# Optimization experiments

Hardware: AMD Instinct MI355X
Metric: run time of the kernel (lower is better)

## Reference

```python
import jax, jax.numpy as jnp
import numpy as np

NUM_HEADS = 4
HIDDEN = 128
LN_EPS = 1e-6
NEG_INF = -1e9


def setup_inputs() -> dict:
    key = jax.random.key(0)
    ks = jax.random.split(key, 8)
    B, S, H, NH = 64, 512, HIDDEN, NUM_HEADS
    enc = jax.random.normal(ks[0], (B, S, H), dtype=jnp.float32)
    mask = jax.random.randint(ks[1], (B, 1, S, S), 0, 2, dtype=jnp.int32)
    scale = 1.0 / np.sqrt(H)
    # torch Linear(H, H*NH, bias=False): weight is (H*NH, H); store transposed (H, H*NH)
    Wq = jax.random.normal(ks[2], (H, H * NH), dtype=jnp.float32) * scale
    Wk = jax.random.normal(ks[3], (H, H * NH), dtype=jnp.float32) * scale
    Wv = jax.random.normal(ks[4], (H, H * NH), dtype=jnp.float32) * scale
    Wo = jax.random.normal(ks[5], (H * NH, H), dtype=jnp.float32) * (1.0 / np.sqrt(H * NH))
    gamma = jnp.ones((H,), dtype=jnp.float32)
    beta = jnp.zeros((H,), dtype=jnp.float32)
    return {"enc": enc, "mask": mask, "Wq": Wq, "Wk": Wk, "Wv": Wv, "Wo": Wo, "gamma": gamma, "beta": beta}


def reference(enc, mask, Wq, Wk, Wv, Wo, gamma, beta):
    B, S, H = enc.shape
    NH = NUM_HEADS
    # projections -> (B, NH, S, H): each head has head_dim == hidden_units
    Q = (enc @ Wq).reshape(B, S, NH, H).transpose(0, 2, 1, 3)
    K = (enc @ Wk).reshape(B, S, NH, H).transpose(0, 2, 1, 3)
    V = (enc @ Wv).reshape(B, S, NH, H).transpose(0, 2, 1, 3)
    # scaled dot-product attention with mask (non-flash: full score matrix)
    scores = jnp.einsum('bhqd,bhkd->bhqk', Q, K) / jnp.sqrt(jnp.float32(H))
    scores = jnp.where(mask == 0, jnp.float32(NEG_INF), scores)
    attn = jax.nn.softmax(scores, axis=-1)  # dropout = identity in eval mode
    ctx = jnp.einsum('bhqk,bhkd->bhqd', attn, V)  # (B, NH, S, H)
    ctx = ctx.transpose(0, 2, 1, 3).reshape(B, S, NH * H)
    out = ctx @ Wo + enc  # dropout identity, residual add
    # LayerNorm over last dim
    mu = jnp.mean(out, axis=-1, keepdims=True)
    var = jnp.var(out, axis=-1, keepdims=True)
    return gamma * (out - mu) / jnp.sqrt(var + LN_EPS) + beta
```

## Files before the change

### kernel.cpp

```cpp
#include <hip/hip_runtime.h>
#include <stdint.h>

#define BATCH 64
#define SLEN 512
#define HID 128
#define NHEAD 4
#define DPROJ 512
#define MTOT (BATCH * SLEN)
#define SCALE 0.08838834764831845f
#define LOG2E 1.4426950408889634f

using short8 = __attribute__((ext_vector_type(8))) short;
using f32x4  = __attribute__((ext_vector_type(4))) float;
using u32x4  = __attribute__((ext_vector_type(4))) unsigned int;
using u32x2  = __attribute__((ext_vector_type(2))) unsigned int;
using us4    = __attribute__((ext_vector_type(4))) unsigned short;

__device__ __forceinline__ unsigned short f2bf(float f) {
  unsigned int u = __float_as_uint(f);
  u += 0x7fffu + ((u >> 16) & 1u);
  return (unsigned short)(u >> 16);
}

__global__ __launch_bounds__(256) void prep_kernel(
    const float* __restrict__ Wq,
    const float* __restrict__ Wk,
    const float* __restrict__ Wv,
    const float* __restrict__ Wo,
    const float* __restrict__ enc,
    const int* __restrict__ mask,
    unsigned short* __restrict__ WT,
    unsigned short* __restrict__ WoT,
    unsigned short* __restrict__ encb,
    unsigned int* __restrict__ mbits)
{
  if (blockIdx.x < 1024) {
    int idx = blockIdx.x * 256 + threadIdx.x;
    int z = idx >> 16;
    int i = idx & 65535;
    if (z < 3) {
      const float* W = (z == 0) ? Wq : (z == 1) ? Wk : Wv;
      float scale = (z == 0) ? (SCALE * LOG2E) : 1.0f;
      int k = i >> 9;
      int n = i & 511;
      WT[(size_t)z * 65536 + (size_t)n * 128 + k] = f2bf(W[i] * scale);
    } else {
      int k = i >> 7;
      int n = i & 127;
      WoT[(size_t)n * 512 + k] = f2bf(Wo[i]);
    }
  } else if (blockIdx.x < 3072) {
    size_t tid = (size_t)(blockIdx.x - 1024) * 256 + threadIdx.x;
    const float* s = enc + tid * 8;
    f32x4 a0 = *(const f32x4*)(s);
    f32x4 a1 = *(const f32x4*)(s + 4);
    short8 v;
    #pragma unroll
    for (int j = 0; j < 4; ++j) v[j] = (short)f2bf(a0[j]);
    #pragma unroll
    for (int j = 0; j < 4; ++j) v[4 + j] = (short)f2bf(a1[j]);
    *(short8*)(encb + tid * 8) = v;
  } else {
    const int l = threadIdx.x & 63;
    size_t wavebase = (size_t)(blockIdx.x - 3072) * 1024 + (threadIdx.x >> 6) * 256;
    unsigned long long b0 = __ballot(mask[wavebase + 0 * 64 + l] != 0);
    unsigned long long b1 = __ballot(mask[wavebase + 1 * 64 + l] != 0);
    unsigned long long b2 = __ballot(mask[wavebase + 2 * 64 + l] != 0);
    unsigned long long b3 = __ballot(mask[wavebase + 3 * 64 + l] != 0);
    if (l < 4) {
      unsigned long long v = (l & 2) ? ((l & 1) ? b3 : b2) : ((l & 1) ? b1 : b0);
      *(unsigned long long*)(mbits + (wavebase >> 5) + l * 2) = v;
    }
  }
}

__global__ __launch_bounds__(256) void qkv_kernel(
    const unsigned short* __restrict__ encb,
    const unsigned short* __restrict__ WT,
    unsigned short* __restrict__ Qh,
    unsigned short* __restrict__ Kh,
    unsigned short* __restrict__ Vt)
{
  const int nt = blockIdx.x;
  const int mt = blockIdx.y;
  const int t = threadIdx.x;
  const int lane = t & 63;
  const int w = t >> 6;
  const int quad = lane >> 4;
  const int l16 = lane & 15;

  __shared__ __align__(16) unsigned short Ald[128 * 136];
  __shared__ __align__(16) unsigned short Bld[128 * 72];

  const int m0 = mt * 128, n0 = nt * 128;
  const int wm = (w >> 1) * 64, wn = (w & 1) * 64;

  #pragma unroll
  for (int i = 0; i < 8; ++i) {
    int idx = i * 256 + t;
    int row = idx >> 4;
    int col = (idx & 15) << 3;
    *(u32x4*)(Ald + row * 136 + col) =
        *(const u32x4*)(encb + (size_t)(m0 + row) * HID + col);
  }

  for (int z = 0; z < 3; ++z) {
    const unsigned short* Wz = WT + (size_t)z * DPROJ * HID;

    f32x4 acc[4][4];
    #pragma unroll
    for (int mi = 0; mi < 4; ++mi)
      #pragma unroll
      for (int ni = 0; ni < 4; ++ni)
        acc[mi][ni] = f32x4{0.f, 0.f, 0.f, 0.f};

    #pragma unroll
    for (int kc = 0; kc < 2; ++kc) {
      __syncthreads();
      #pragma unroll
      for (int i = 0; i < 4; ++i) {
        int idx = i * 256 + t;
        int row = idx >> 3;
        int col = (idx & 7) << 3;
        *(u32x4*)(Bld + row * 72 + col) =
            *(const u32x4*)(Wz + (size_t)(n0 + row) * HID + kc * 64 + col);
      }
      __syncthreads();

      #pragma unroll
      for (int kk = 0; kk < 2; ++kk) {
        short8 a[4], bb[4];
        #pragma unroll
        for (int mi = 0; mi < 4; ++mi)
          a[mi] = *(const short8*)(Ald + (wm + mi * 16 + l16) * 136 + kc * 64 + kk * 32 + quad * 8);
        #pragma unroll
        for (int ni = 0; ni < 4; ++ni)
          bb[ni] = *(const short8*)(Bld + (wn + ni * 16 + l16) * 72 + kk * 32 + quad * 8);
        if (z < 2) {
          #pragma unroll
          for (int mi = 0; mi < 4; ++mi)
            #pragma unroll
            for (int ni = 0; ni < 4; ++ni)
              acc[mi][ni] = __builtin_amdgcn_mfma_f32_16x16x32_bf16(bb[ni], a[mi], acc[mi][ni], 0, 0, 0);
        } else {
          #pragma unroll
          for (int mi = 0; mi < 4; ++mi)
            #pragma unroll
            for (int ni = 0; ni < 4; ++ni)
              acc[mi][ni] = __builtin_amdgcn_mfma_f32_16x16x32_bf16(a[mi], bb[ni], acc[mi][ni], 0, 0, 0);
        }
      }
    }

    if (z < 2) {
      unsigned short* outz = ((z == 0) ? Qh : Kh) + (size_t)nt * MTOT * HID;
      #pragma unroll
      for (int mi = 0; mi < 4; ++mi)
        #pragma unroll
        for (int ni = 0; ni < 4; ++ni) {
          int m = m0 + wm + mi * 16 + l16;
          int dbase = wn + ni * 16 + quad * 4;
          us4 pk;
          #pragma unroll
          for (int r = 0; r < 4; ++r) pk[r] = f2bf(acc[mi][ni][r]);
          *(us4*)(outz + (size_t)m * HID + dbase) = pk;
        }
    } else {
      #pragma unroll
      for (int mi = 0; mi < 4; ++mi)
        #pragma unroll
        for (int ni = 0; ni < 4; ++ni) {
          int row0 = m0 + wm + mi * 16 + quad * 4;
          int b = row0 >> 9, s = row0 & 511;
          int d = wn + ni * 16 + l16;
          us4 pk;
          #pragma unroll
          for (int r = 0; r < 4; ++r) pk[r] = f2bf(acc[mi][ni][r]);
          *(us4*)(Vt + ((size_t)(nt * BATCH + b) * HID + d) * SLEN + s) = pk;
        }
    }
  }
}

__global__ __launch_bounds__(512, 4) void attn_kernel(
    const unsigned short* __restrict__ Qh,
    const unsigned short* __restrict__ Kh,
    const unsigned short* __restrict__ Vt,
    const unsigned int* __restrict__ mbits,
    unsigned short* __restrict__ ctx)
{
  const int lin = blockIdx.x;
  const int work = (lin & 7) * 128 + (lin >> 3);
  const int qt = work & 3;
  const int h  = (work >> 2) & 3;
  const int b  = work >> 4;

  const int t = threadIdx.x;
  const int lane = t & 63;
  const int w = t >> 6;
  const int quad = lane >> 4;
  const int l16 = lane & 15;

  __shared__ __align__(16) unsigned short Kld[2][64 * 136];
  __shared__ __align__(16) unsigned short Vtld[2][128 * 72];

  const int q0 = qt * 128;
  const size_t rowbase = (size_t)b * SLEN;
  const unsigned short* kbase0 = Kh + ((size_t)h * MTOT + rowbase) * HID;
  const unsigned short* vbase  = Vt + (size_t)(h * BATCH + b) * HID * SLEN;
  const unsigned int* mrow = mbits + (size_t)b * SLEN * 16;

  const int k_key = t >> 4, k_col = (t & 15) << 3;
  const int v_d   = t >> 3, v_cc  = (t & 7) << 3;

  short8 qa[4];
  {
    const unsigned short* qbase =
        Qh + ((size_t)h * MTOT + rowbase + q0 + w * 16 + l16) * HID + quad * 8;
    #pragma unroll
    for (int kk = 0; kk < 4; ++kk)
      qa[kk] = *(const short8*)(qbase + kk * 32);
  }

  short8 ones;
  #pragma unroll
  for (int j = 0; j < 8; ++j) ones[j] = (short)0x3F80;

  f32x4 oc[8], oc9;
  #pragma unroll
  for (int nd = 0; nd < 8; ++nd) oc[nd] = f32x4{0.f, 0.f, 0.f, 0.f};
  oc9 = f32x4{0.f, 0.f, 0.f, 0.f};

  const unsigned int* mq = mrow + (size_t)(q0 + w * 16 + l16) * 16;

  u32x4 kreg[2], vreg[2];
  #pragma unroll
  for (int i = 0; i < 2; ++i) {
    kreg[i] = *(const u32x4*)(kbase0 + (size_t)(k_key + i * 32) * HID + k_col);
    vreg[i] = *(const u32x4*)(vbase + (size_t)(v_d + i * 64) * SLEN + v_cc);
  }
  #pragma unroll
  for (int i = 0; i < 2; ++i) {
    *(u32x4*)(Kld[0] + (k_key + i * 32) * 136 + k_col) = kreg[i];
    *(u32x4*)(Vtld[0] + (v_d + i * 64) * 72 + v_cc) = vreg[i];
  }
  #pragma unroll
  for (int i = 0; i < 2; ++i) {
    kreg[i] = *(const u32x4*)(kbase0 + (size_t)(64 + k_key + i * 32) * HID + k_col);
    vreg[i] = *(const u32x4*)(vbase + (size_t)(v_d + i * 64) * SLEN + 64 + v_cc);
  }
  asm volatile("s_waitcnt lgkmcnt(0)" ::: "memory");
  __builtin_amdgcn_s_barrier();

  for (int c0 = 0; c0 < SLEN; c0 += 64) {
    const int p = (c0 >> 6) & 1;
    const unsigned short* Kr = Kld[p];
    const unsigned short* Vr = Vtld[p];

    if (c0 + 64 < SLEN) {
      unsigned short* Kw = Kld[p ^ 1];
      unsigned short* Vw = Vtld[p ^ 1];
      #pragma unroll
      for (int i = 0; i < 2; ++i) {
        *(u32x4*)(Kw + (k_key + i * 32) * 136 + k_col) = kreg[i];
        *(u32x4*)(Vw + (v_d + i * 64) * 72 + v_cc) = vreg[i];
      }
      if (c0 + 128 < SLEN) {
        #pragma unroll
        for (int i = 0; i < 2; ++i) {
          kreg[i] = *(const u32x4*)(kbase0 + (size_t)(c0 + 128 + k_key + i * 32) * HID + k_col);
          vreg[i] = *(const u32x4*)(vbase + (size_t)(v_d + i * 64) * SLEN + c0 + 128 + v_cc);
        }
      }
    }

    u32x2 mw = *(const u32x2*)(mq + (c0 >> 5));

    f32x4 sc[4];
    #pragma unroll
    for (int ni = 0; ni < 4; ++ni) sc[ni] = f32x4{0.f, 0.f, 0.f, 0.f};
    __builtin_amdgcn_s_setprio(1);
    #pragma unroll
    for (int kk = 0; kk < 4; ++kk) {
      #pragma unroll
      for (int ni = 0; ni < 4; ++ni) {
        short8 bb = *(const short8*)(Kr + (ni * 16 + l16) * 136 + kk * 32 + quad * 8);
        sc[ni] = __builtin_amdgcn_mfma_f32_16x16x32_bf16(bb, qa[kk], sc[ni], 0, 0, 0);
      }
    }
    __builtin_amdgcn_s_setprio(0);

    unsigned int pk[4][2];
    #pragma unroll
    for (int ni = 0; ni < 4; ++ni) {
      unsigned wsel = (ni < 2) ? mw[0] : mw[1];
      float pp[4];
      #pragma unroll
      for (int r = 0; r < 4; ++r) {
        int bit = (ni & 1) * 16 + quad * 4 + r;
        float e = __builtin_amdgcn_exp2f(sc[ni][r]);
        pp[r] = ((wsel >> bit) & 1u) ? e : 0.f;
      }
      asm("v_cvt_pk_bf16_f32 %0, %1, %2" : "=v"(pk[ni][0]) : "v"(pp[0]), "v"(pp[1]));
      asm("v_cvt_pk_bf16_f32 %0, %1, %2" : "=v"(pk[ni][1]) : "v"(pp[2]), "v"(pp[3]));
    }

    #pragma unroll
    for (int kb = 0; kb < 2; ++kb) {
      unsigned int c0w = pk[kb * 2][0], c2w = pk[kb * 2 + 1][0];
      asm("v_permlane32_swap_b32 %0, %1" : "+v"(c0w), "+v"(c2w));
      asm("v_permlane16_swap_b32 %0, %1" : "+v"(c0w), "+v"(c2w));
      unsigned int c1w = pk[kb * 2][1], c3w = pk[kb * 2 + 1][1];
      asm("v_permlane32_swap_b32 %0, %1" : "+v"(c1w), "+v"(c3w));
      asm("v_permlane16_swap_b32 %0, %1" : "+v"(c1w), "+v"(c3w));
      short8 a = __builtin_bit_cast(short8, u32x4{c0w, c1w, c2w, c3w});
      __builtin_amdgcn_s_setprio(1);
      #pragma unroll
      for (int nd = 0; nd < 8; ++nd) {
        short8 bv = *(const short8*)(Vr + (nd * 16 + l16) * 72 + kb * 32 + quad * 8);
        oc[nd] = __builtin_amdgcn_mfma_f32_16x16x32_bf16(a, bv, oc[nd], 0, 0, 0);
      }
      oc9 = __builtin_amdgcn_mfma_f32_16x16x32_bf16(a, ones, oc9, 0, 0, 0);
      __builtin_amdgcn_s_setprio(0);
    }

    if (c0 + 64 < SLEN) {
      asm volatile("s_waitcnt lgkmcnt(0)" ::: "memory");
      __builtin_amdgcn_s_barrier();
    }
  }

  float rcp[4];
  #pragma unroll
  for (int r = 0; r < 4; ++r) rcp[r] = __builtin_amdgcn_rcpf(oc9[r]);
  #pragma unroll
  for (int nd = 0; nd < 8; ++nd)
    #pragma unroll
    for (int r = 0; r < 4; ++r) {
      float val = oc[nd][r] * rcp[r];
      int row = q0 + w * 16 + quad * 4 + r;
      int col = h * HID + nd * 16 + l16;
      ctx[(rowbase + row) * DPROJ + col] = f2bf(val);
    }
}

__global__ __launch_bounds__(256, 4) void oproj_ln_kernel(
    const unsigned short* __restrict__ ctx,
    const unsigned short* __restrict__ WoT,
    const float* __restrict__ enc,
    const float* __restrict__ gamma,
    const float* __restrict__ beta,
    float* __restrict__ out)
{
  const int m0 = blockIdx.x * 64;
  const int t = threadIdx.x;
  const int lane = t & 63;
  const int w = t >> 6;
  const int quad = lane >> 4;
  const int l16 = lane & 15;

  __shared__ __align__(16) unsigned short Actx[64 * 72];
  __shared__ __align__(16) unsigned short Bw[128 * 72];

  f32x4 acc[8];
  #pragma unroll
  for (int ni = 0; ni < 8; ++ni) acc[ni] = f32x4{0.f, 0.f, 0.f, 0.f};

  for (int kc = 0; kc < DPROJ; kc += 64) {
    __syncthreads();
    #pragma unroll
    for (int i = 0; i < 2; ++i) {
      int idx = i * 256 + t;
      int row = idx >> 3;
      int col = (idx & 7) << 3;
      *(u32x4*)(Actx + row * 72 + col) =
          *(const u32x4*)(ctx + (size_t)(m0 + row) * DPROJ + kc + col);
    }
    #pragma unroll
    for (int i = 0; i < 4; ++i) {
      int idx = i * 256 + t;
      int row = idx >> 3;
      int col = (idx & 7) << 3;
      *(u32x4*)(Bw + row * 72 + col) =
          *(const u32x4*)(WoT + (size_t)row * DPROJ + kc + col);
    }
    __syncthreads();
    #pragma unroll
    for (int kk = 0; kk < 2; ++kk) {
      short8 a = *(const short8*)(Actx + (w * 16 + l16) * 72 + kk * 32 + quad * 8);
      #pragma unroll
      for (int ni = 0; ni < 8; ++ni) {
        short8 bb = *(const short8*)(Bw + (ni * 16 + l16) * 72 + kk * 32 + quad * 8);
        acc[ni] = __builtin_amdgcn_mfma_f32_16x16x32_bf16(a, bb, acc[ni], 0, 0, 0);
      }
    }
  }

  float g[8], be[8];
  #pragma unroll
  for (int ni = 0; ni < 8; ++ni) {
    g[ni] = gamma[ni * 16 + l16];
    be[ni] = beta[ni * 16 + l16];
  }

  float val[8][4];
  #pragma unroll
  for (int r = 0; r < 4; ++r) {
    int m = m0 + w * 16 + quad * 4 + r;
    const float* erow = enc + (size_t)m * HID;
    float s = 0.f, s2 = 0.f;
    #pragma unroll
    for (int ni = 0; ni < 8; ++ni) {
      float v = acc[ni][r] + erow[ni * 16 + l16];
      val[ni][r] = v;
      s += v;
      s2 += v * v;
    }
    #pragma unroll
    for (int off = 1; off < 16; off <<= 1) {
      s  += __shfl_xor(s, off, 64);
      s2 += __shfl_xor(s2, off, 64);
    }
    float mean = s * (1.f / 128.f);
    float var = s2 * (1.f / 128.f) - mean * mean;
    float rstd = rsqrtf(var + 1e-6f);
    float* orow = out + (size_t)m * HID;
    #pragma unroll
    for (int ni = 0; ni < 8; ++ni)
      orow[ni * 16 + l16] = g[ni] * (val[ni][r] - mean) * rstd + be[ni];
  }
}

extern "C" void kernel_launch(void* const* d_in, const int* in_sizes, int n_in,
                              void* d_out, int out_size, void* d_ws, size_t ws_size,
                              hipStream_t stream) {
  const float* enc   = (const float*)d_in[0];
  const int*   mask  = (const int*)d_in[1];
  const float* Wq    = (const float*)d_in[2];
  const float* Wk    = (const float*)d_in[3];
  const float* Wv    = (const float*)d_in[4];
  const float* Wo    = (const float*)d_in[5];
  const float* gamma = (const float*)d_in[6];
  const float* beta  = (const float*)d_in[7];
  float* out = (float*)d_out;

  unsigned short* WT  = (unsigned short*)d_ws;
  unsigned short* WoT = WT + (size_t)3 * DPROJ * HID;
  unsigned short* Qh  = WoT + (size_t)HID * DPROJ;
  unsigned short* Kh  = Qh + (size_t)NHEAD * MTOT * HID;
  unsigned short* Vt  = Kh + (size_t)NHEAD * MTOT * HID;
  unsigned short* ctx = Vt + (size_t)NHEAD * MTOT * HID;
  unsigned short* encb = ctx + (size_t)MTOT * DPROJ;
  unsigned int* mbits = (unsigned int*)(encb + (size_t)MTOT * HID * 2);

  prep_kernel<<<19456, 256, 0, stream>>>(Wq, Wk, Wv, Wo, enc, mask, WT, WoT, encb, mbits);
  qkv_kernel<<<dim3(4, 256), 256, 0, stream>>>(encb, WT, Qh, Kh, Vt);
  attn_kernel<<<1024, 512, 0, stream>>>(Qh, Kh, Vt, mbits, ctx);
  oproj_ln_kernel<<<MTOT / 64, 256, 0, stream>>>(ctx, WoT, enc, gamma, beta, out);
}
```

Before: 228.4 us.

## Double-buffer weight and context tiles in QKV and output-projection GEMMs

Both the QKV projection and the output-projection/LayerNorm kernels now prefetch the next K-chunk from global memory into registers while the current chunk is consumed. The next chunk is then written to a second LDS buffer, so each step needs one barrier instead of two. In the QKV kernel the three Q/K/V passes are flattened into a single six-step pipeline. The goal is to hide global-load latency behind MFMA work, at the cost of extra registers and LDS. The output kernel's launch-bounds occupancy hint drops from 4 to 2 to make room for this.

```diff
diff --git a/kernel.cpp b/kernel.cpp
--- a/kernel.cpp
+++ b/kernel.cpp
@@ -90,94 +90,121 @@
   const int l16 = lane & 15;
 
   __shared__ __align__(16) unsigned short Ald[128 * 136];
-  __shared__ __align__(16) unsigned short Bld[128 * 72];
+  __shared__ __align__(16) unsigned short Bld[2][128 * 72];
 
   const int m0 = mt * 128, n0 = nt * 128;
   const int wm = (w >> 1) * 64, wn = (w & 1) * 64;
 
-  #pragma unroll
-  for (int i = 0; i < 8; ++i) {
-    int idx = i * 256 + t;
-    int row = idx >> 4;
-    int col = (idx & 15) << 3;
-    *(u32x4*)(Ald + row * 136 + col) =
-        *(const u32x4*)(encb + (size_t)(m0 + row) * HID + col);
-  }
-
-  for (int z = 0; z < 3; ++z) {
-    const unsigned short* Wz = WT + (size_t)z * DPROJ * HID;
-
-    f32x4 acc[4][4];
-    #pragma unroll
-    for (int mi = 0; mi < 4; ++mi)
+  const int b_row = t >> 3, b_col = (t & 7) << 3;
+
+  {
+    u32x4 areg[8];
+    #pragma unroll
+    for (int i = 0; i < 8; ++i) {
+      int idx = i * 256 + t;
+      areg[i] = *(const u32x4*)(encb + (size_t)(m0 + (idx >> 4)) * HID + ((idx & 15) << 3));
+    }
+    u32x4 breg0[4];
+    #pragma unroll
+    for (int i = 0; i < 4; ++i)
+      breg0[i] = *(const u32x4*)(WT + (size_t)(n0 + b_row + i * 32) * HID + b_col);
+    #pragma unroll
+    for (int i = 0; i < 8; ++i) {
+      int idx = i * 256 + t;
+      *(u32x4*)(Ald + (idx >> 4) * 136 + ((idx & 15) << 3)) = areg[i];
+    }
+    #pragma unroll
+    for (int i = 0; i < 4; ++i)
+      *(u32x4*)(Bld[0] + (b_row + i * 32) * 72 + b_col) = breg0[i];
+  }
+  u32x4 breg[4];
+  #pragma unroll
+  for (int i = 0; i < 4; ++i)
+    breg[i] = *(const u32x4*)(WT + (size_t)(n0 + b_row + i * 32) * HID + 64 + b_col);
+  asm volatile("s_waitcnt lgkmcnt(0)" ::: "memory");
+  __builtin_amdgcn_s_barrier();
+
+  f32x4 acc[4][4];
+  #pragma unroll
+  for (int s = 0; s < 6; ++s) {
+    const int z = s >> 1, kc = s & 1, p = s & 1;
+    if (kc == 0) {
+      #pragma unroll
+      for (int mi = 0; mi < 4; ++mi)
+        #pragma unroll
+        for (int ni = 0; ni < 4; ++ni)
+          acc[mi][ni] = f32x4{0.f, 0.f, 0.f, 0.f};
+    }
+
+    const unsigned short* Br = Bld[p];
+    #pragma unroll
+    for (int kk = 0; kk < 2; ++kk) {
+      short8 a[4], bb[4];
+      #pragma unroll
+      for (int mi = 0; mi < 4; ++mi)
+        a[mi] = *(const short8*)(Ald + (wm + mi * 16 + l16) * 136 + kc * 64 + kk * 32 + quad * 8);
       #pragma unroll
       for (int ni = 0; ni < 4; ++ni)
-        acc[mi][ni] = f32x4{0.f, 0.f, 0.f, 0.f};
-
-    #pragma unroll
-    for (int kc = 0; kc < 2; ++kc) {
-      __syncthreads();
-      #pragma unroll
-      for (int i = 0; i < 4; ++i) {
-        int idx = i * 256 + t;
-        int row = idx >> 3;
-        int col = (idx & 7) << 3;
-        *(u32x4*)(Bld + row * 72 + col) =
-            *(const u32x4*)(Wz + (size_t)(n0 + row) * HID + kc * 64 + col);
-      }
-      __syncthreads();
-
-      #pragma unroll
-      for (int kk = 0; kk < 2; ++kk) {
-        short8 a[4], bb[4];
+        bb[ni] = *(const short8*)(Br + (wn + ni * 16 + l16) * 72 + kk * 32 + quad * 8);
+      if (z < 2) {
         #pragma unroll
         for (int mi = 0; mi < 4; ++mi)
-          a[mi] = *(const short8*)(Ald + (wm + mi * 16 + l16) * 136 + kc * 64 + kk * 32 + quad * 8);
-        #pragma unroll
-        for (int ni = 0; ni < 4; ++ni)
-          bb[ni] = *(const short8*)(Bld + (wn + ni * 16 + l16) * 72 + kk * 32 + quad * 8);
-        if (z < 2) {
           #pragma unroll
-          for (int mi = 0; mi < 4; ++mi)
+          for (int ni = 0; ni < 4; ++ni)
+            acc[mi][ni] = __builtin_amdgcn_mfma_f32_16x16x32_bf16(bb[ni], a[mi], acc[mi][ni], 0, 0, 0);
+      } else {
+        #pragma unroll
+        for (int mi = 0; mi < 4; ++mi)
+          #pragma unroll
+          for (int ni = 0; ni < 4; ++ni)
+            acc[mi][ni] = __builtin_amdgcn_mfma_f32_16x16x32_bf16(a[mi], bb[ni], acc[mi][ni], 0, 0, 0);
+      }
+    }
+
+    if (s < 5) {
+      unsigned short* Bw2 = Bld[p ^ 1];
+      #pragma unroll
+      for (int i = 0; i < 4; ++i)
+        *(u32x4*)(Bw2 + (b_row + i * 32) * 72 + b_col) = breg[i];
+      if (s < 4) {
+        const int s2 = s + 2;
+        const unsigned short* Wz = WT + (size_t)(s2 >> 1) * DPROJ * HID;
+        #pragma unroll
+        for (int i = 0; i < 4; ++i)
+          breg[i] = *(const u32x4*)(Wz + (size_t)(n0 + b_row + i * 32) * HID + (s2 & 1) * 64 + b_col);
+      }
+      asm volatile("s_waitcnt lgkmcnt(0)" ::: "memory");
+      __builtin_amdgcn_s_barrier();
+    }
+
+    if (kc == 1) {
+      if (z < 2) {
+        unsigned short* outz = ((z == 0) ? Qh : Kh) + (size_t)nt * MTOT * HID;
+        #pragma unroll
+        for (int mi = 0; mi < 4; ++mi)
+          #pragma unroll
+          for (int ni = 0; ni < 4; ++ni) {
+            int m = m0 + wm + mi * 16 + l16;
+            int dbase = wn + ni * 16 + quad * 4;
+            us4 pk;
             #pragma unroll
-            for (int ni = 0; ni < 4; ++ni)
-              acc[mi][ni] = __builtin_amdgcn_mfma_f32_16x16x32_bf16(bb[ni], a[mi], acc[mi][ni], 0, 0, 0);
-        } else {
+            for (int r = 0; r < 4; ++r) pk[r] = f2bf(acc[mi][ni][r]);
+            *(us4*)(outz + (size_t)m * HID + dbase) = pk;
+          }
+      } else {
+        #pragma unroll
+        for (int mi = 0; mi < 4; ++mi)
           #pragma unroll
-          for (int mi = 0; mi < 4; ++mi)
+          for (int ni = 0; ni < 4; ++ni) {
+            int row0 = m0 + wm + mi * 16 + quad * 4;
+            int b = row0 >> 9, sres = row0 & 511;
+            int d = wn + ni * 16 + l16;
+            us4 pk;
             #pragma unroll
-            for (int ni = 0; ni < 4; ++ni)
-              acc[mi][ni] = __builtin_amdgcn_mfma_f32_16x16x32_bf16(a[mi], bb[ni], acc[mi][ni], 0, 0, 0);
-        }
-      }
-    }
-
-    if (z < 2) {
-      unsigned short* outz = ((z == 0) ? Qh : Kh) + (size_t)nt * MTOT * HID;
-      #pragma unroll
-      for (int mi = 0; mi < 4; ++mi)
-        #pragma unroll
-        for (int ni = 0; ni < 4; ++ni) {
-          int m = m0 + wm + mi * 16 + l16;
-          int dbase = wn + ni * 16 + quad * 4;
-          us4 pk;
-          #pragma unroll
-          for (int r = 0; r < 4; ++r) pk[r] = f2bf(acc[mi][ni][r]);
-          *(us4*)(outz + (size_t)m * HID + dbase) = pk;
-        }
-    } else {
-      #pragma unroll
-      for (int mi = 0; mi < 4; ++mi)
-        #pragma unroll
-        for (int ni = 0; ni < 4; ++ni) {
-          int row0 = m0 + wm + mi * 16 + quad * 4;
-          int b = row0 >> 9, s = row0 & 511;
-          int d = wn + ni * 16 + l16;
-          us4 pk;
-          #pragma unroll
-          for (int r = 0; r < 4; ++r) pk[r] = f2bf(acc[mi][ni][r]);
-          *(us4*)(Vt + ((size_t)(nt * BATCH + b) * HID + d) * SLEN + s) = pk;
-        }
+            for (int r = 0; r < 4; ++r) pk[r] = f2bf(acc[mi][ni][r]);
+            *(us4*)(Vt + ((size_t)(nt * BATCH + b) * HID + d) * SLEN + sres) = pk;
+          }
+      }
     }
   }
 }
@@ -344,7 +371,7 @@
     }
 }
 
-__global__ __launch_bounds__(256, 4) void oproj_ln_kernel(
+__global__ __launch_bounds__(256, 2) void oproj_ln_kernel(
     const unsigned short* __restrict__ ctx,
     const unsigned short* __restrict__ WoT,
     const float* __restrict__ enc,
@@ -359,40 +386,72 @@
   const int quad = lane >> 4;
   const int l16 = lane & 15;
 
-  __shared__ __align__(16) unsigned short Actx[64 * 72];
-  __shared__ __align__(16) unsigned short Bw[128 * 72];
+  __shared__ __align__(16) unsigned short Actx[2][64 * 72];
+  __shared__ __align__(16) unsigned short Bw[2][128 * 72];
+
+  const int a_row = t >> 3, a_col = (t & 7) << 3;
+  const int b_row = t >> 3, b_col = (t & 7) << 3;
 
   f32x4 acc[8];
   #pragma unroll
   for (int ni = 0; ni < 8; ++ni) acc[ni] = f32x4{0.f, 0.f, 0.f, 0.f};
 
-  for (int kc = 0; kc < DPROJ; kc += 64) {
-    __syncthreads();
-    #pragma unroll
-    for (int i = 0; i < 2; ++i) {
-      int idx = i * 256 + t;
-      int row = idx >> 3;
-      int col = (idx & 7) << 3;
-      *(u32x4*)(Actx + row * 72 + col) =
-          *(const u32x4*)(ctx + (size_t)(m0 + row) * DPROJ + kc + col);
-    }
-    #pragma unroll
-    for (int i = 0; i < 4; ++i) {
-      int idx = i * 256 + t;
-      int row = idx >> 3;
-      int col = (idx & 7) << 3;
-      *(u32x4*)(Bw + row * 72 + col) =
-          *(const u32x4*)(WoT + (size_t)row * DPROJ + kc + col);
-    }
-    __syncthreads();
+  u32x4 areg[2], breg[4];
+  #pragma unroll
+  for (int i = 0; i < 2; ++i)
+    areg[i] = *(const u32x4*)(ctx + (size_t)(m0 + a_row + i * 32) * DPROJ + a_col);
+  #pragma unroll
+  for (int i = 0; i < 4; ++i)
+    breg[i] = *(const u32x4*)(WoT + (size_t)(b_row + i * 32) * DPROJ + b_col);
+  #pragma unroll
+  for (int i = 0; i < 2; ++i)
+    *(u32x4*)(Actx[0] + (a_row + i * 32) * 72 + a_col) = areg[i];
+  #pragma unroll
+  for (int i = 0; i < 4; ++i)
+    *(u32x4*)(Bw[0] + (b_row + i * 32) * 72 + b_col) = breg[i];
+  #pragma unroll
+  for (int i = 0; i < 2; ++i)
+    areg[i] = *(const u32x4*)(ctx + (size_t)(m0 + a_row + i * 32) * DPROJ + 64 + a_col);
+  #pragma unroll
+  for (int i = 0; i < 4; ++i)
+    breg[i] = *(const u32x4*)(WoT + (size_t)(b_row + i * 32) * DPROJ + 64 + b_col);
+  asm volatile("s_waitcnt lgkmcnt(0)" ::: "memory");
+  __builtin_amdgcn_s_barrier();
+
+  #pragma unroll
+  for (int it = 0; it < 8; ++it) {
+    const int p = it & 1;
+    const unsigned short* Ar = Actx[p];
+    const unsigned short* Br = Bw[p];
     #pragma unroll
     for (int kk = 0; kk < 2; ++kk) {
-      short8 a = *(const short8*)(Actx + (w * 16 + l16) * 72 + kk * 32 + quad * 8);
+      short8 a = *(const short8*)(Ar + (w * 16 + l16) * 72 + kk * 32 + quad * 8);
       #pragma unroll
       for (int ni = 0; ni < 8; ++ni) {
-        short8 bb = *(const short8*)(Bw + (ni * 16 + l16) * 72 + kk * 32 + quad * 8);
+        short8 bb = *(const short8*)(Br + (ni * 16 + l16) * 72 + kk * 32 + quad * 8);
         acc[ni] = __builtin_amdgcn_mfma_f32_16x16x32_bf16(a, bb, acc[ni], 0, 0, 0);
       }
+    }
+    if (it < 7) {
+      unsigned short* Aw2 = Actx[p ^ 1];
+      unsigned short* Bw2 = Bw[p ^ 1];
+      #pragma unroll
+      for (int i = 0; i < 2; ++i)
+        *(u32x4*)(Aw2 + (a_row + i * 32) * 72 + a_col) = areg[i];
+      #pragma unroll
+      for (int i = 0; i < 4; ++i)
+        *(u32x4*)(Bw2 + (b_row + i * 32) * 72 + b_col) = breg[i];
+      if (it < 6) {
+        const int kc2 = (it + 2) * 64;
+        #pragma unroll
+        for (int i = 0; i < 2; ++i)
+          areg[i] = *(const u32x4*)(ctx + (size_t)(m0 + a_row + i * 32) * DPROJ + kc2 + a_col);
+        #pragma unroll
+        for (int i = 0; i < 4; ++i)
+          breg[i] = *(const u32x4*)(WoT + (size_t)(b_row + i * 32) * DPROJ + kc2 + b_col);
+      }
+      asm volatile("s_waitcnt lgkmcnt(0)" ::: "memory");
+      __builtin_amdgcn_s_barrier();
     }
   }
 
```

Measured after the change: 222.9 us. 1.02x faster.
